# Kernel tuning notes

Measured on AMD Instinct MI355X. Metric: run time of the kernel, lower is better.

Reference implementation:

```python
import jax, jax.numpy as jnp
import numpy as np

IN_DIM = 63
WIDTH = 256
OUT_DIM = 256
NUM_LAYERS = 8
SKIP = {4}
N_POINTS = 524288


def _layer_dims():
    dims = []
    for i in range(NUM_LAYERS - 1):
        if i == 0:
            dims.append((IN_DIM, WIDTH))
        elif i in SKIP:
            dims.append((WIDTH + IN_DIM, WIDTH))
        else:
            dims.append((WIDTH, WIDTH))
    dims.append((WIDTH, OUT_DIM))
    return dims


def setup_inputs() -> dict:
    key = jax.random.key(0)
    keys = jax.random.split(key, 2 * NUM_LAYERS + 1)
    inp = {"in_tensor": jax.random.normal(keys[0], (N_POINTS, IN_DIM), dtype=jnp.float32)}
    for i, (fan_in, fan_out) in enumerate(_layer_dims()):
        scale = 1.0 / np.sqrt(fan_in)
        inp[f"W{i}"] = jax.random.uniform(keys[1 + 2 * i], (fan_in, fan_out), jnp.float32, -scale, scale)
        inp[f"b{i}"] = jax.random.uniform(keys[2 + 2 * i], (fan_out,), jnp.float32, -scale, scale)
    return inp


def reference(in_tensor, W0, b0, W1, b1, W2, b2, W3, b3, W4, b4, W5, b5, W6, b6, W7, b7):
    Ws = [W0, W1, W2, W3, W4, W5, W6, W7]
    bs = [b0, b1, b2, b3, b4, b5, b6, b7]
    x = in_tensor
    for i in range(NUM_LAYERS):
        if i in SKIP:
            x = jnp.concatenate([in_tensor, x], axis=-1)  # [N, in_dim+width]
        x = x @ Ws[i] + bs[i]
        if i < NUM_LAYERS - 1:
            x = jax.nn.relu(x)
    # out_activation is None
    return x
```

## Files before the change

kernel.cpp:

```cpp
#include <hip/hip_runtime.h>
#include <cstddef>


typedef _Float16 half8 __attribute__((ext_vector_type(8)));
typedef _Float16 half4 __attribute__((ext_vector_type(4)));
typedef float floatx4 __attribute__((ext_vector_type(4)));

#define N_POINTS 524288
#define IN_DIM   63
#define P_TILE   128
#define N_BLOCKS (N_POINTS / P_TILE)


__global__ void mlp_prep(_Float16* __restrict__ Wp,
    const float* __restrict__ W0, const float* __restrict__ W1,
    const float* __restrict__ W2, const float* __restrict__ W3,
    const float* __restrict__ W4, const float* __restrict__ W5,
    const float* __restrict__ W6, const float* __restrict__ W7)
{
    int e    = blockIdx.x * 256 + threadIdx.x;
    int gks  = e >> 13;
    int rem  = e & 8191;
    int mt   = rem >> 9;
    int r3   = rem & 511;
    int lane = r3 >> 3;
    int i    = r3 & 7;
    int m    = mt * 16 + (lane & 15);

    int l, kb;
    if      (gks <  2) { l = 0; kb = gks;      }
    else if (gks < 10) { l = 1; kb = gks - 2;  }
    else if (gks < 18) { l = 2; kb = gks - 10; }
    else if (gks < 26) { l = 3; kb = gks - 18; }
    else if (gks < 36) { l = 4; kb = gks - 26; }
    else if (gks < 44) { l = 5; kb = gks - 36; }
    else if (gks < 52) { l = 6; kb = gks - 44; }
    else               { l = 7; kb = gks - 52; }
    int k = kb * 32 + (lane >> 4) * 8 + i;

    const float* W = (l==0)?W0:(l==1)?W1:(l==2)?W2:(l==3)?W3:(l==4)?W4:(l==5)?W5:(l==6)?W6:W7;
    float v;
    if (l == 0)      v = (k < IN_DIM) ? W[k * 256 + m] : 0.f;
    else if (l == 4) v = (k < IN_DIM) ? W[k * 256 + m]
                        : (k == IN_DIM ? 0.f : W[(k - 1) * 256 + m]);
    else             v = W[k * 256 + m];
    Wp[e] = (_Float16)v;
}

__device__ __forceinline__ void a_frags(const _Float16* __restrict__ Wp,
                                        int gks, int wv, int lane, half8 (&a)[4])
{
    const _Float16* base = Wp + ((size_t)gks * 16 + (size_t)wv * 4) * 512 + lane * 8;
#pragma unroll
    for (int mt = 0; mt < 4; ++mt)
        a[mt] = *(const half8*)(base + mt * 512);
}

__device__ __forceinline__ void b_frags(const _Float16* __restrict__ src,
                                        int rowHalfs, int cbase, int ln, int q,
                                        half8 (&b)[8])
{
    int ch = ((cbase + q) ^ (ln & 7)) << 3;
    const _Float16* base = src + ln * rowHalfs + ch;
    int step = 16 * rowHalfs;
#pragma unroll
    for (int nt = 0; nt < 8; ++nt)
        b[nt] = *(const half8*)(base + nt * step);
}

__device__ __forceinline__ void mfma_step(const half8 (&a)[4], const half8 (&b)[8],
                                          floatx4 (&acc)[4][8])
{
#pragma unroll
    for (int nt = 0; nt < 8; ++nt)
#pragma unroll
        for (int mt = 0; mt < 4; ++mt)
            acc[mt][nt] = __builtin_amdgcn_mfma_f32_16x16x32_f16(a[mt], b[nt], acc[mt][nt], 0, 0, 0);
}

template<int KS, int KS_IN, bool RELU, bool LAST>
__device__ __forceinline__ void layer_fn(const _Float16* __restrict__ Wp, int gbase,
                                         const float* __restrict__ bias,
                                         const _Float16* __restrict__ inL,
                                         _Float16* __restrict__ actL,
                                         float* __restrict__ out, int pbase,
                                         int wv, int lane)
{
    const int ln = lane & 15, q = lane >> 4;
    floatx4 acc[4][8];
#pragma unroll
    for (int mt = 0; mt < 4; ++mt)
#pragma unroll
        for (int nt = 0; nt < 8; ++nt)
            acc[mt][nt] = (floatx4){0.f, 0.f, 0.f, 0.f};

#pragma unroll 2
    for (int s = 0; s < KS_IN; ++s) {
        half8 a[4]; a_frags(Wp, gbase + s, wv, lane, a);
        half8 b[8]; b_frags(inL, 64, s * 4, ln, q, b);
        mfma_step(a, b, acc);
    }
#pragma unroll 2
    for (int s = 0; s < KS - KS_IN; ++s) {
        half8 a[4]; a_frags(Wp, gbase + KS_IN + s, wv, lane, a);
        half8 b[8]; b_frags(actL, 256, s * 4, ln, q, b);
        mfma_step(a, b, acc);
    }

    floatx4 bv[4];
#pragma unroll
    for (int mt = 0; mt < 4; ++mt)
        bv[mt] = *(const floatx4*)(bias + wv * 64 + mt * 16 + q * 4);

    if (!LAST) __syncthreads();

#pragma unroll
    for (int mt = 0; mt < 4; ++mt) {
#pragma unroll
        for (int nt = 0; nt < 8; ++nt) {
            floatx4 v = acc[mt][nt];
            v.x += bv[mt].x; v.y += bv[mt].y; v.z += bv[mt].z; v.w += bv[mt].w;
            if (RELU) {
                v.x = fmaxf(v.x, 0.f); v.y = fmaxf(v.y, 0.f);
                v.z = fmaxf(v.z, 0.f); v.w = fmaxf(v.w, 0.f);
            }
            if (LAST) {
                size_t p = (size_t)(pbase + nt * 16 + ln);
                *(floatx4*)(out + p * 256 + wv * 64 + mt * 16 + q * 4) = v;
            } else {
                half4 h = { (_Float16)v.x, (_Float16)v.y, (_Float16)v.z, (_Float16)v.w };
                int c  = wv * 8 + mt * 2 + (q >> 1);
                int ch = c ^ (ln & 7);
                *(half4*)(actL + (nt * 16 + ln) * 256 + ch * 8 + (q & 1) * 4) = h;
            }
        }
    }
    if (!LAST) __syncthreads();
}

__global__ void __launch_bounds__(256, 2) mlp_main(
    const float* __restrict__ in, const _Float16* __restrict__ Wp,
    const float* __restrict__ b0, const float* __restrict__ b1,
    const float* __restrict__ b2, const float* __restrict__ b3,
    const float* __restrict__ b4, const float* __restrict__ b5,
    const float* __restrict__ b6, const float* __restrict__ b7,
    float* __restrict__ out)
{
    __shared__ __align__(16) _Float16 actL[128 * 256];
    __shared__ __align__(16) _Float16 inL [128 * 64];

    const int t = threadIdx.x;
    const int wv = t >> 6, lane = t & 63;
    const int pbase = blockIdx.x * P_TILE;

#pragma unroll 4
    for (int idx = t; idx < 128 * 64; idx += 256) {
        int p = idx >> 6, f = idx & 63;
        float v = (f < IN_DIM) ? in[(size_t)(pbase + p) * IN_DIM + f] : 0.f;
        inL[p * 64 + (((f >> 3) ^ (p & 7)) << 3) + (f & 7)] = (_Float16)v;
    }
    __syncthreads();

    layer_fn< 2, 2, true,  false>(Wp,  0, b0, inL, actL, out, pbase, wv, lane);
    layer_fn< 8, 0, true,  false>(Wp,  2, b1, inL, actL, out, pbase, wv, lane);
    layer_fn< 8, 0, true,  false>(Wp, 10, b2, inL, actL, out, pbase, wv, lane);
    layer_fn< 8, 0, true,  false>(Wp, 18, b3, inL, actL, out, pbase, wv, lane);
    layer_fn<10, 2, true,  false>(Wp, 26, b4, inL, actL, out, pbase, wv, lane);
    layer_fn< 8, 0, true,  false>(Wp, 36, b5, inL, actL, out, pbase, wv, lane);
    layer_fn< 8, 0, true,  false>(Wp, 44, b6, inL, actL, out, pbase, wv, lane);
    layer_fn< 8, 0, false, true >(Wp, 52, b7, inL, actL, out, pbase, wv, lane);
}

extern "C" void kernel_launch(void* const* d_in, const int* in_sizes, int n_in,
                              void* d_out, int out_size, void* d_ws, size_t ws_size,
                              hipStream_t stream)
{
    const float* in = (const float*)d_in[0];
    const float* W[8]; const float* B[8];
    for (int i = 0; i < 8; ++i) {
        W[i] = (const float*)d_in[1 + 2 * i];
        B[i] = (const float*)d_in[2 + 2 * i];
    }
    _Float16* Wp = (_Float16*)d_ws;

    hipLaunchKernelGGL(mlp_prep, dim3(1920), dim3(256), 0, stream,
                       Wp, W[0], W[1], W[2], W[3], W[4], W[5], W[6], W[7]);
    hipLaunchKernelGGL(mlp_main, dim3(N_BLOCKS), dim3(256), 0, stream,
                       in, Wp, B[0], B[1], B[2], B[3], B[4], B[5], B[6], B[7],
                       (float*)d_out);
}
```

Measured before the change: 1.131 ms.

## Halve point tile to 64, raise occupancy, and prefetch weight fragments

```diff
diff --git a/kernel.cpp b/kernel.cpp
--- a/kernel.cpp
+++ b/kernel.cpp
@@ -8,7 +8,7 @@
 
 #define N_POINTS 524288
 #define IN_DIM   63
-#define P_TILE   128
+#define P_TILE   64
 #define N_BLOCKS (N_POINTS / P_TILE)
 
 
@@ -58,24 +58,14 @@
 
 __device__ __forceinline__ void b_frags(const _Float16* __restrict__ src,
                                         int rowHalfs, int cbase, int ln, int q,
-                                        half8 (&b)[8])
+                                        half8 (&b)[4])
 {
     int ch = ((cbase + q) ^ (ln & 7)) << 3;
     const _Float16* base = src + ln * rowHalfs + ch;
     int step = 16 * rowHalfs;
 #pragma unroll
-    for (int nt = 0; nt < 8; ++nt)
+    for (int nt = 0; nt < 4; ++nt)
         b[nt] = *(const half8*)(base + nt * step);
-}
-
-__device__ __forceinline__ void mfma_step(const half8 (&a)[4], const half8 (&b)[8],
-                                          floatx4 (&acc)[4][8])
-{
-#pragma unroll
-    for (int nt = 0; nt < 8; ++nt)
-#pragma unroll
-        for (int mt = 0; mt < 4; ++mt)
-            acc[mt][nt] = __builtin_amdgcn_mfma_f32_16x16x32_f16(a[mt], b[nt], acc[mt][nt], 0, 0, 0);
 }
 
 template<int KS, int KS_IN, bool RELU, bool LAST>
@@ -87,24 +77,33 @@
                                          int wv, int lane)
 {
     const int ln = lane & 15, q = lane >> 4;
-    floatx4 acc[4][8];
+    floatx4 acc[4][4];
 #pragma unroll
     for (int mt = 0; mt < 4; ++mt)
 #pragma unroll
-        for (int nt = 0; nt < 8; ++nt)
+        for (int nt = 0; nt < 4; ++nt)
             acc[mt][nt] = (floatx4){0.f, 0.f, 0.f, 0.f};
 
+    half8 a_cur[4], a_nxt[4];
+    a_frags(Wp, gbase, wv, lane, a_cur);
+
 #pragma unroll 2
-    for (int s = 0; s < KS_IN; ++s) {
-        half8 a[4]; a_frags(Wp, gbase + s, wv, lane, a);
-        half8 b[8]; b_frags(inL, 64, s * 4, ln, q, b);
-        mfma_step(a, b, acc);
-    }
-#pragma unroll 2
-    for (int s = 0; s < KS - KS_IN; ++s) {
-        half8 a[4]; a_frags(Wp, gbase + KS_IN + s, wv, lane, a);
-        half8 b[8]; b_frags(actL, 256, s * 4, ln, q, b);
-        mfma_step(a, b, acc);
+    for (int s = 0; s < KS; ++s) {
+        int sn = (s + 1 < KS) ? s + 1 : s;
+        a_frags(Wp, gbase + sn, wv, lane, a_nxt);
+
+        half8 b[4];
+        if (s < KS_IN) b_frags(inL, 64, s * 4, ln, q, b);
+        else           b_frags(actL, 256, (s - KS_IN) * 4, ln, q, b);
+
+#pragma unroll
+        for (int nt = 0; nt < 4; ++nt)
+#pragma unroll
+            for (int mt = 0; mt < 4; ++mt)
+                acc[mt][nt] = __builtin_amdgcn_mfma_f32_16x16x32_f16(a_cur[mt], b[nt], acc[mt][nt], 0, 0, 0);
+
+#pragma unroll
+        for (int mt = 0; mt < 4; ++mt) a_cur[mt] = a_nxt[mt];
     }
 
     floatx4 bv[4];
@@ -117,7 +116,7 @@
 #pragma unroll
     for (int mt = 0; mt < 4; ++mt) {
 #pragma unroll
-        for (int nt = 0; nt < 8; ++nt) {
+        for (int nt = 0; nt < 4; ++nt) {
             floatx4 v = acc[mt][nt];
             v.x += bv[mt].x; v.y += bv[mt].y; v.z += bv[mt].z; v.w += bv[mt].w;
             if (RELU) {
@@ -138,7 +137,7 @@
     if (!LAST) __syncthreads();
 }
 
-__global__ void __launch_bounds__(256, 2) mlp_main(
+__global__ void __launch_bounds__(256, 4) mlp_main(
     const float* __restrict__ in, const _Float16* __restrict__ Wp,
     const float* __restrict__ b0, const float* __restrict__ b1,
     const float* __restrict__ b2, const float* __restrict__ b3,
@@ -146,15 +145,15 @@
     const float* __restrict__ b6, const float* __restrict__ b7,
     float* __restrict__ out)
 {
-    __shared__ __align__(16) _Float16 actL[128 * 256];
-    __shared__ __align__(16) _Float16 inL [128 * 64];
+    __shared__ __align__(16) _Float16 actL[P_TILE * 256];
+    __shared__ __align__(16) _Float16 inL [P_TILE * 64];
 
     const int t = threadIdx.x;
     const int wv = t >> 6, lane = t & 63;
     const int pbase = blockIdx.x * P_TILE;
 
 #pragma unroll 4
-    for (int idx = t; idx < 128 * 64; idx += 256) {
+    for (int idx = t; idx < P_TILE * 64; idx += 256) {
         int p = idx >> 6, f = idx & 63;
         float v = (f < IN_DIM) ? in[(size_t)(pbase + p) * IN_DIM + f] : 0.f;
         inL[p * 64 + (((f >> 3) ^ (p & 7)) << 3) + (f & 7)] = (_Float16)v;
```

New measurement: 1.031 ms. 1.1x faster.
